# Kernel optimization log

Measured on AMD Instinct MI355X. Metric: run time of the kernel, lower is better.

Reference implementation:

```python
import jax, jax.numpy as jnp
import numpy as np

D_MODEL = 1024
D_INTERNAL = 64
SEQ = 2048
BATCH = 4


def setup_inputs() -> dict:
    key = jax.random.key(0)
    ks = jax.random.split(key, 9)
    s = 1.0 / np.sqrt(D_MODEL)
    return {
        "query": jax.random.normal(ks[0], (SEQ, BATCH, D_MODEL), jnp.float32),
        "key": jax.random.normal(ks[1], (SEQ, BATCH, D_MODEL), jnp.float32),
        "value": jax.random.normal(ks[2], (SEQ, BATCH, D_MODEL), jnp.float32),
        "Wq": jax.random.normal(ks[3], (D_MODEL, D_INTERNAL), jnp.float32) * s,
        "bq": jnp.zeros((D_INTERNAL,), jnp.float32),
        "Wk": jax.random.normal(ks[4], (D_MODEL, D_INTERNAL), jnp.float32) * s,
        "bk": jnp.zeros((D_INTERNAL,), jnp.float32),
        "Wv": jax.random.normal(ks[5], (D_MODEL, D_MODEL), jnp.float32) * s,
        "bv": jnp.zeros((D_MODEL,), jnp.float32),
    }


def reference(query, key, value, Wq, bq, Wk, bk, Wv, bv):
    # inputs: (S, B, D); project then move batch first -> (B, S, *)
    q = (query @ Wq + bq).transpose(1, 0, 2)          # (B, S, d_int)
    k = (key @ Wk + bk).transpose(1, 0, 2)            # (B, S, d_int)
    v = (value @ Wv + bv).transpose(1, 0, 2)          # (B, S, D)
    scores = jnp.einsum("bqd,bkd->bqk", q, k) / jnp.sqrt(jnp.float32(D_INTERNAL))
    probs = jax.nn.softmax(scores, axis=-1)           # row softmax over keys
    # extra renormalization over the QUERY axis (dim=1), as in the source
    probs = probs / (1e-9 + probs.sum(axis=1, keepdims=True))
    aten = jnp.einsum("bqk,bkd->bqd", probs, v).transpose(1, 0, 2)  # (S, B, D)
    return aten, probs
```

## Files before the change

### kernel.cpp

```cpp
#include <hip/hip_runtime.h>
#include <math.h>

#define SEQ 2048
#define BATCH 4
#define DM 1024
#define DI 64

typedef __attribute__((ext_vector_type(8))) short bf16x8;
typedef __attribute__((ext_vector_type(4))) float f32x4;

__device__ __forceinline__ unsigned short f2bf(float f) {
  unsigned u = __float_as_uint(f);
  unsigned r = (u + 0x7fff + ((u >> 16) & 1)) >> 16;
  return (unsigned short)r;
}

__device__ __forceinline__ void gload_lds16(const void* g, void* l) {
  __builtin_amdgcn_global_load_lds(
      (const __attribute__((address_space(1))) unsigned int*)g,
      (__attribute__((address_space(3))) unsigned int*)l, 16, 0, 0);
}


__global__ __launch_bounds__(256) void wqkt_kernel(
    const float* __restrict__ Wq, const float* __restrict__ Wk,
    unsigned short* __restrict__ WqkT) {
  __shared__ unsigned short t[64][65];
  const float* W = blockIdx.y ? Wk : Wq;
  unsigned short* WT = WqkT + (size_t)blockIdx.y * DI * DM;
  int bx = blockIdx.x * 64;
  int lx = threadIdx.x & 63, ly = threadIdx.x >> 6;
#pragma unroll
  for (int i = 0; i < 64; i += 4)
    t[ly + i][lx] = f2bf(W[(size_t)(bx + ly + i) * DI + lx]);
  __syncthreads();
#pragma unroll
  for (int i = 0; i < 64; i += 4)
    WT[(size_t)(ly + i) * DM + bx + lx] = t[lx][ly + i];
}

__global__ __launch_bounds__(256) void wvt_kernel(
    const float* __restrict__ W, unsigned short* __restrict__ WT) {
  __shared__ unsigned short t[64][65];
  int bx = blockIdx.x * 64, by = blockIdx.y * 64;
  int lx = threadIdx.x & 63, ly = threadIdx.x >> 6;
#pragma unroll
  for (int i = 0; i < 64; i += 4)
    t[ly + i][lx] = f2bf(W[(size_t)(bx + ly + i) * DM + by + lx]);
  __syncthreads();
#pragma unroll
  for (int i = 0; i < 64; i += 4)
    WT[(size_t)(by + ly + i) * DM + bx + lx] = t[lx][ly + i];
}

__global__ __launch_bounds__(256) void qkproj_mfma(
    const float* __restrict__ query, const float* __restrict__ key,
    const unsigned short* __restrict__ WqkT,
    const float* __restrict__ bq, const float* __restrict__ bk,
    unsigned short* __restrict__ qbf, unsigned short* __restrict__ kbf) {
  __shared__ __align__(16) unsigned short As[32 * 32];
  __shared__ __align__(16) unsigned short Bs[64 * 32];
  int which = blockIdx.y;
  const float* A = (which ? key : query) + (size_t)blockIdx.x * 32 * DM;
  const unsigned short* Bt = WqkT + (size_t)which * DI * DM;
  const float* bias = which ? bk : bq;
  unsigned short* outp = which ? kbf : qbf;

  const int tid = threadIdx.x;
  const int lane = tid & 63, wave = tid >> 6;
  const int lrow = lane & 15, quad = lane >> 4;
  const int wr = (wave >> 1) * 16;
  const int wc = (wave & 1) * 32;
  const int sw = (quad ^ ((lrow >> 1) & 3)) * 8;
  f32x4 acc[2] = {};

  const int am = tid >> 3, asub = tid & 7;
  const int akc = asub * 4;
  const int asl = am * 32 + (((asub >> 1) ^ ((am >> 1) & 3)) * 8) + (asub & 1) * 4;
  const int bn = tid >> 2;
  const int bkc = (((tid & 3) ^ ((bn >> 1) & 3)) * 8);

  for (int k0 = 0; k0 < DM; k0 += 32) {
    __syncthreads();
    gload_lds16(Bt + (size_t)bn * DM + k0 + bkc, Bs + wave * 512);
    float4 a = *(const float4*)(A + (size_t)am * DM + k0 + akc);
    ushort4 h;
    h.x = f2bf(a.x); h.y = f2bf(a.y); h.z = f2bf(a.z); h.w = f2bf(a.w);
    *(ushort4*)&As[asl] = h;
    __syncthreads();
    bf16x8 af = *(const bf16x8*)&As[(wr + lrow) * 32 + sw];
    bf16x8 b0 = *(const bf16x8*)&Bs[(wc + lrow) * 32 + sw];
    bf16x8 b1 = *(const bf16x8*)&Bs[(wc + 16 + lrow) * 32 + sw];
    acc[0] = __builtin_amdgcn_mfma_f32_16x16x32_bf16(af, b0, acc[0], 0, 0, 0);
    acc[1] = __builtin_amdgcn_mfma_f32_16x16x32_bf16(af, b1, acc[1], 0, 0, 0);
  }
  int sbase = blockIdx.x * 8 + (wr >> 2) + quad;
#pragma unroll
  for (int ni = 0; ni < 2; ++ni) {
    int n = wc + ni * 16 + lrow;
    float bb = bias[n];
#pragma unroll
    for (int reg = 0; reg < 4; ++reg)
      outp[((size_t)reg * SEQ + sbase) * DI + n] = f2bf(acc[ni][reg] + bb);
  }
}

__global__ __launch_bounds__(256) void vcast_kernel(
    const float* __restrict__ value, unsigned short* __restrict__ vbf) {
  size_t i = ((size_t)blockIdx.x * 256 + threadIdx.x) * 8;
  float4 a = *(const float4*)(value + i);
  float4 b = *(const float4*)(value + i + 4);
  bf16x8 h;
  h[0] = (short)f2bf(a.x); h[1] = (short)f2bf(a.y);
  h[2] = (short)f2bf(a.z); h[3] = (short)f2bf(a.w);
  h[4] = (short)f2bf(b.x); h[5] = (short)f2bf(b.y);
  h[6] = (short)f2bf(b.z); h[7] = (short)f2bf(b.w);
  *(bf16x8*)(vbf + i) = h;
}

__device__ __forceinline__ void mfma_core_bb(
    const unsigned short* __restrict__ At, int lda,
    const unsigned short* __restrict__ Bt, int ldb,
    int K, f32x4 (&acc)[4][4],
    unsigned short* As, unsigned short* Bs) {
  const int tid  = threadIdx.x;
  const int lane = tid & 63;
  const int wave = tid >> 6;
  const int wr   = (wave >> 1) * 64;
  const int wc   = (wave & 1) * 64;
  const int lrow = lane & 15;
  const int quad = lane >> 4;
  const int sw   = (quad ^ ((lrow >> 1) & 3)) * 8;

  for (int k0 = 0; k0 < K; k0 += 32) {
    __syncthreads();
#pragma unroll
    for (int it = 0; it < 2; ++it) {
      int c = it * 256 + wave * 64 + lane;
      int m = c >> 2, kc = ((c & 3) ^ ((c >> 3) & 3)) * 8;
      gload_lds16(At + (size_t)m * lda + k0 + kc,
                  As + (size_t)(it * 256 + wave * 64) * 8);
    }
#pragma unroll
    for (int it = 0; it < 2; ++it) {
      int c = it * 256 + wave * 64 + lane;
      int n = c >> 2, kc = ((c & 3) ^ ((c >> 3) & 3)) * 8;
      gload_lds16(Bt + (size_t)n * ldb + k0 + kc,
                  Bs + (size_t)(it * 256 + wave * 64) * 8);
    }
    __syncthreads();
    bf16x8 af[4], bfr[4];
#pragma unroll
    for (int mi = 0; mi < 4; ++mi)
      af[mi] = *(const bf16x8*)&As[(wr + mi * 16 + lrow) * 32 + sw];
#pragma unroll
    for (int ni = 0; ni < 4; ++ni)
      bfr[ni] = *(const bf16x8*)&Bs[(wc + ni * 16 + lrow) * 32 + sw];
#pragma unroll
    for (int mi = 0; mi < 4; ++mi)
#pragma unroll
      for (int ni = 0; ni < 4; ++ni)
        acc[mi][ni] = __builtin_amdgcn_mfma_f32_16x16x32_bf16(
            af[mi], bfr[ni], acc[mi][ni], 0, 0, 0);
  }
}

__device__ __forceinline__ void mfma_core_bb_12864(
    const unsigned short* __restrict__ At, int lda,
    const unsigned short* __restrict__ Bt, int ldb,
    int K, f32x4 (&acc)[4][2],
    unsigned short* As, unsigned short* Bs) {
  const int tid  = threadIdx.x;
  const int lane = tid & 63;
  const int wave = tid >> 6;
  const int wr   = (wave >> 1) * 64;
  const int wc   = (wave & 1) * 32;
  const int lrow = lane & 15;
  const int quad = lane >> 4;
  const int sw   = (quad ^ ((lrow >> 1) & 3)) * 8;
  const int bn   = tid >> 2;
  const int bkc  = ((tid & 3) ^ ((bn >> 1) & 3)) * 8;

  for (int k0 = 0; k0 < K; k0 += 32) {
    __syncthreads();
#pragma unroll
    for (int it = 0; it < 2; ++it) {
      int c = it * 256 + tid;
      int m = c >> 2, kc = ((c & 3) ^ ((m >> 1) & 3)) * 8;
      gload_lds16(At + (size_t)m * lda + k0 + kc,
                  As + (size_t)(it * 256 + wave * 64) * 8);
    }
    gload_lds16(Bt + (size_t)bn * ldb + k0 + bkc, Bs + wave * 512);
    __syncthreads();
    bf16x8 af[4], bfr[2];
#pragma unroll
    for (int mi = 0; mi < 4; ++mi)
      af[mi] = *(const bf16x8*)&As[(wr + mi * 16 + lrow) * 32 + sw];
#pragma unroll
    for (int ni = 0; ni < 2; ++ni)
      bfr[ni] = *(const bf16x8*)&Bs[(wc + ni * 16 + lrow) * 32 + sw];
#pragma unroll
    for (int mi = 0; mi < 4; ++mi)
#pragma unroll
      for (int ni = 0; ni < 2; ++ni)
        acc[mi][ni] = __builtin_amdgcn_mfma_f32_16x16x32_bf16(
            af[mi], bfr[ni], acc[mi][ni], 0, 0, 0);
  }
}

__global__ __launch_bounds__(256) void vproj_mfma(
    const unsigned short* __restrict__ vbf, const unsigned short* __restrict__ WvT,
    const float* __restrict__ bv, unsigned short* __restrict__ vT) {
  __shared__ __align__(16) unsigned short As[128 * 32];
  __shared__ __align__(16) unsigned short Bs[64 * 32];
  __shared__ __align__(16) unsigned short ep[64 * 4 * 32];
  f32x4 acc[4][2] = {};
  int m0 = blockIdx.x * 128, n0 = blockIdx.y * 64;
  mfma_core_bb_12864(vbf + (size_t)m0 * DM, DM, WvT + (size_t)n0 * DM, DM, DM,
                     acc, As, Bs);
  const int tid = threadIdx.x;
  const int lane = tid & 63, wave = tid >> 6;
  const int wr = (wave >> 1) * 64, wc = (wave & 1) * 32;
  const int lrow = lane & 15, quad = lane >> 4;
#pragma unroll
  for (int mi = 0; mi < 4; ++mi) {
    int ss = (wr >> 2) + mi * 4 + quad;
#pragma unroll
    for (int ni = 0; ni < 2; ++ni) {
      int nn = wc + ni * 16 + lrow;
      float bias = bv[n0 + nn];
      int swz = (nn & 3) << 3;
#pragma unroll
      for (int reg = 0; reg < 4; ++reg)
        ep[nn * 128 + reg * 32 + (ss ^ swz)] = f2bf(acc[mi][ni][reg] + bias);
    }
  }
  __syncthreads();
  int s0 = m0 >> 2;
#pragma unroll
  for (int t8 = 0; t8 < 4; ++t8) {
    int c = t8 * 256 + tid;
    int ss8 = (c & 3) * 8, b = (c >> 2) & 3, nn = c >> 4;
    uint4 vv = *(const uint4*)&ep[nn * 128 + b * 32 + (ss8 ^ ((nn & 3) << 3))];
    *(uint4*)&vT[((size_t)(b * DM + n0 + nn)) * SEQ + s0 + ss8] = vv;
  }
}

__global__ __launch_bounds__(256) void scores_mfma(
    const unsigned short* __restrict__ qbf, const unsigned short* __restrict__ kbf,
    float* __restrict__ probs) {
  __shared__ __align__(16) unsigned short As[128 * 32];
  __shared__ __align__(16) unsigned short Bs[128 * 32];
  int b = blockIdx.z;
  f32x4 acc[4][4] = {};
  mfma_core_bb(qbf + ((size_t)b * SEQ + blockIdx.x * 128) * DI, DI,
               kbf + ((size_t)b * SEQ + blockIdx.y * 128) * DI, DI, DI,
               acc, As, Bs);
  float* C = probs + (size_t)b * SEQ * SEQ;
  const int lane = threadIdx.x & 63, wave = threadIdx.x >> 6;
  const int wr = (wave >> 1) * 64, wc = (wave & 1) * 64;
  const int lrow = lane & 15, quad = lane >> 4;
#pragma unroll
  for (int mi = 0; mi < 4; ++mi) {
    int qr = blockIdx.x * 128 + wr + mi * 16 + quad * 4;
#pragma unroll
    for (int ni = 0; ni < 4; ++ni) {
      int n = blockIdx.y * 128 + wc + ni * 16 + lrow;
#pragma unroll
      for (int reg = 0; reg < 4; ++reg)
        C[(size_t)(qr + reg) * SEQ + n] = acc[mi][ni][reg] * 0.125f;
    }
  }
}

__global__ __launch_bounds__(256) void softmax_kernel(float* __restrict__ probs) {
  size_t row = (size_t)blockIdx.y * SEQ + blockIdx.x;
  float* p = probs + row * SEQ;
  int tid = threadIdx.x;
  float4 x0 = *(float4*)(p + tid * 4);
  float4 x1 = *(float4*)(p + 1024 + tid * 4);
  float m = fmaxf(fmaxf(fmaxf(x0.x, x0.y), fmaxf(x0.z, x0.w)),
                  fmaxf(fmaxf(x1.x, x1.y), fmaxf(x1.z, x1.w)));
  __shared__ float red[256];
  red[tid] = m;
  __syncthreads();
  for (int s2 = 128; s2 > 0; s2 >>= 1) {
    if (tid < s2) red[tid] = fmaxf(red[tid], red[tid + s2]);
    __syncthreads();
  }
  m = red[0];
  __syncthreads();
  x0.x = __expf(x0.x - m); x0.y = __expf(x0.y - m);
  x0.z = __expf(x0.z - m); x0.w = __expf(x0.w - m);
  x1.x = __expf(x1.x - m); x1.y = __expf(x1.y - m);
  x1.z = __expf(x1.z - m); x1.w = __expf(x1.w - m);
  float sum = x0.x + x0.y + x0.z + x0.w + x1.x + x1.y + x1.z + x1.w;
  red[tid] = sum;
  __syncthreads();
  for (int s2 = 128; s2 > 0; s2 >>= 1) {
    if (tid < s2) red[tid] += red[tid + s2];
    __syncthreads();
  }
  float inv = 1.0f / red[0];
  x0.x *= inv; x0.y *= inv; x0.z *= inv; x0.w *= inv;
  x1.x *= inv; x1.y *= inv; x1.z *= inv; x1.w *= inv;
  *(float4*)(p + tid * 4) = x0;
  *(float4*)(p + 1024 + tid * 4) = x1;
}

__global__ void zero_kernel(float* __restrict__ p, int n) {
  int i = blockIdx.x * blockDim.x + threadIdx.x;
  if (i < n) p[i] = 0.f;
}

__global__ __launch_bounds__(256) void colsum_kernel(
    const float* __restrict__ probs, float* __restrict__ colsum) {
  int b = blockIdx.z;
  int k = blockIdx.x * 256 + threadIdx.x;
  int q0 = blockIdx.y * 128;
  const float* p = probs + (size_t)b * SEQ * SEQ + (size_t)q0 * SEQ + k;
  float sum = 0.f;
#pragma unroll 4
  for (int i = 0; i < 128; ++i) sum += p[(size_t)i * SEQ];
  atomicAdd(&colsum[b * SEQ + k], sum);
}

__global__ void invcol_kernel(const float* __restrict__ colsum,
                              float* __restrict__ invcol, int n) {
  int i = blockIdx.x * blockDim.x + threadIdx.x;
  if (i < n) invcol[i] = 1.0f / (1e-9f + colsum[i]);
}

__global__ __launch_bounds__(256) void renorm_kernel(
    float* __restrict__ probs, const float* __restrict__ invcol,
    unsigned short* __restrict__ smb) {
  size_t i4 = (size_t)blockIdx.x * blockDim.x + threadIdx.x;
  size_t f = i4 * 4;
  int b = (int)(f >> 22);
  int k = (int)(f & 2047);
  float4 p = *(float4*)(probs + f);
  float4 c = *(const float4*)(invcol + b * SEQ + k);
  p.x *= c.x; p.y *= c.y; p.z *= c.z; p.w *= c.w;
  *(float4*)(probs + f) = p;
  ushort4 h;
  h.x = f2bf(p.x); h.y = f2bf(p.y); h.z = f2bf(p.z); h.w = f2bf(p.w);
  *(ushort4*)(smb + f) = h;
}

__global__ __launch_bounds__(256) void aten_mfma(
    const unsigned short* __restrict__ smb, const unsigned short* __restrict__ vT,
    float* __restrict__ out) {
  __shared__ __align__(16) unsigned short As[128 * 32];
  __shared__ __align__(16) unsigned short Bs[128 * 32];
  int b = blockIdx.z;
  f32x4 acc[4][4] = {};
  int m0 = blockIdx.x * 128, n0 = blockIdx.y * 128;
  mfma_core_bb(smb + ((size_t)b * SEQ + m0) * SEQ, SEQ,
               vT + ((size_t)b * DM + n0) * SEQ, SEQ, SEQ, acc, As, Bs);
  const int lane = threadIdx.x & 63, wave = threadIdx.x >> 6;
  const int wr = (wave >> 1) * 64, wc = (wave & 1) * 64;
  const int lrow = lane & 15, quad = lane >> 4;
#pragma unroll
  for (int mi = 0; mi < 4; ++mi) {
    int qr = m0 + wr + mi * 16 + quad * 4;
#pragma unroll
    for (int ni = 0; ni < 4; ++ni) {
      int n = n0 + wc + ni * 16 + lrow;
#pragma unroll
      for (int reg = 0; reg < 4; ++reg)
        out[(size_t)(qr + reg) * (BATCH * DM) + b * DM + n] = acc[mi][ni][reg];
    }
  }
}

extern "C" void kernel_launch(void* const* d_in, const int* in_sizes, int n_in,
                              void* d_out, int out_size, void* d_ws, size_t ws_size,
                              hipStream_t stream) {
  const float* query = (const float*)d_in[0];
  const float* key   = (const float*)d_in[1];
  const float* value = (const float*)d_in[2];
  const float* Wq    = (const float*)d_in[3];
  const float* bq    = (const float*)d_in[4];
  const float* Wk    = (const float*)d_in[5];
  const float* bk    = (const float*)d_in[6];
  const float* Wv    = (const float*)d_in[7];
  const float* bv    = (const float*)d_in[8];

  float* out   = (float*)d_out;
  float* probs = out + (size_t)SEQ * BATCH * DM;

  unsigned short* WvT  = (unsigned short*)d_ws;
  unsigned short* WqkT = WvT  + (size_t)DM * DM;
  unsigned short* qbf  = WqkT + (size_t)2 * DI * DM;
  unsigned short* kbf  = qbf  + (size_t)BATCH * SEQ * DI;
  unsigned short* vT   = kbf  + (size_t)BATCH * SEQ * DI;
  unsigned short* smb  = vT   + (size_t)BATCH * DM * SEQ;
  unsigned short* vbf  = smb;
  float* colsum = (float*)(smb + (size_t)BATCH * SEQ * SEQ);
  float* invcol = colsum + (size_t)BATCH * SEQ;

  wqkt_kernel<<<dim3(16, 2), 256, 0, stream>>>(Wq, Wk, WqkT);
  qkproj_mfma<<<dim3(SEQ * BATCH / 32, 2), 256, 0, stream>>>(
      query, key, WqkT, bq, bk, qbf, kbf);
  wvt_kernel<<<dim3(16, 16), 256, 0, stream>>>(Wv, WvT);
  vcast_kernel<<<(SEQ * BATCH * DM / 8) / 256, 256, 0, stream>>>(value, vbf);
  vproj_mfma<<<dim3(SEQ * BATCH / 128, DM / 64), 256, 0, stream>>>(vbf, WvT, bv, vT);
  scores_mfma<<<dim3(SEQ / 128, SEQ / 128, BATCH), 256, 0, stream>>>(qbf, kbf, probs);
  softmax_kernel<<<dim3(SEQ, BATCH), 256, 0, stream>>>(probs);
  zero_kernel<<<(BATCH * SEQ + 255) / 256, 256, 0, stream>>>(colsum, BATCH * SEQ);
  colsum_kernel<<<dim3(SEQ / 256, SEQ / 128, BATCH), 256, 0, stream>>>(probs, colsum);
  invcol_kernel<<<(BATCH * SEQ + 255) / 256, 256, 0, stream>>>(colsum, invcol, BATCH * SEQ);
  renorm_kernel<<<(BATCH * SEQ * SEQ / 4) / 256, 256, 0, stream>>>(probs, invcol, smb);
  aten_mfma<<<dim3(SEQ / 128, DM / 128, BATCH), 256, 0, stream>>>(smb, vT, out);
}
```

Before: 351.5 us.

## Fuse softmax exp and row sums into scores kernel, defer row normalization

```diff
diff --git a/kernel.cpp b/kernel.cpp
--- a/kernel.cpp
+++ b/kernel.cpp
@@ -248,7 +248,7 @@
 
 __global__ __launch_bounds__(256) void scores_mfma(
     const unsigned short* __restrict__ qbf, const unsigned short* __restrict__ kbf,
-    float* __restrict__ probs) {
+    float* __restrict__ probs, float* __restrict__ rowsum) {
   __shared__ __align__(16) unsigned short As[128 * 32];
   __shared__ __align__(16) unsigned short Bs[128 * 32];
   int b = blockIdx.z;
@@ -257,55 +257,42 @@
                kbf + ((size_t)b * SEQ + blockIdx.y * 128) * DI, DI, DI,
                acc, As, Bs);
   float* C = probs + (size_t)b * SEQ * SEQ;
+  float* rs = rowsum + (size_t)b * SEQ;
   const int lane = threadIdx.x & 63, wave = threadIdx.x >> 6;
   const int wr = (wave >> 1) * 64, wc = (wave & 1) * 64;
   const int lrow = lane & 15, quad = lane >> 4;
 #pragma unroll
   for (int mi = 0; mi < 4; ++mi) {
     int qr = blockIdx.x * 128 + wr + mi * 16 + quad * 4;
+    float r0 = 0.f, r1 = 0.f, r2 = 0.f, r3 = 0.f;
 #pragma unroll
     for (int ni = 0; ni < 4; ++ni) {
       int n = blockIdx.y * 128 + wc + ni * 16 + lrow;
-#pragma unroll
-      for (int reg = 0; reg < 4; ++reg)
-        C[(size_t)(qr + reg) * SEQ + n] = acc[mi][ni][reg] * 0.125f;
-    }
-  }
-}
-
-__global__ __launch_bounds__(256) void softmax_kernel(float* __restrict__ probs) {
-  size_t row = (size_t)blockIdx.y * SEQ + blockIdx.x;
-  float* p = probs + row * SEQ;
-  int tid = threadIdx.x;
-  float4 x0 = *(float4*)(p + tid * 4);
-  float4 x1 = *(float4*)(p + 1024 + tid * 4);
-  float m = fmaxf(fmaxf(fmaxf(x0.x, x0.y), fmaxf(x0.z, x0.w)),
-                  fmaxf(fmaxf(x1.x, x1.y), fmaxf(x1.z, x1.w)));
-  __shared__ float red[256];
-  red[tid] = m;
-  __syncthreads();
-  for (int s2 = 128; s2 > 0; s2 >>= 1) {
-    if (tid < s2) red[tid] = fmaxf(red[tid], red[tid + s2]);
-    __syncthreads();
-  }
-  m = red[0];
-  __syncthreads();
-  x0.x = __expf(x0.x - m); x0.y = __expf(x0.y - m);
-  x0.z = __expf(x0.z - m); x0.w = __expf(x0.w - m);
-  x1.x = __expf(x1.x - m); x1.y = __expf(x1.y - m);
-  x1.z = __expf(x1.z - m); x1.w = __expf(x1.w - m);
-  float sum = x0.x + x0.y + x0.z + x0.w + x1.x + x1.y + x1.z + x1.w;
-  red[tid] = sum;
-  __syncthreads();
-  for (int s2 = 128; s2 > 0; s2 >>= 1) {
-    if (tid < s2) red[tid] += red[tid + s2];
-    __syncthreads();
-  }
-  float inv = 1.0f / red[0];
-  x0.x *= inv; x0.y *= inv; x0.z *= inv; x0.w *= inv;
-  x1.x *= inv; x1.y *= inv; x1.z *= inv; x1.w *= inv;
-  *(float4*)(p + tid * 4) = x0;
-  *(float4*)(p + 1024 + tid * 4) = x1;
+      float e0 = __expf(acc[mi][ni][0] * 0.125f);
+      float e1 = __expf(acc[mi][ni][1] * 0.125f);
+      float e2 = __expf(acc[mi][ni][2] * 0.125f);
+      float e3 = __expf(acc[mi][ni][3] * 0.125f);
+      C[(size_t)(qr + 0) * SEQ + n] = e0;
+      C[(size_t)(qr + 1) * SEQ + n] = e1;
+      C[(size_t)(qr + 2) * SEQ + n] = e2;
+      C[(size_t)(qr + 3) * SEQ + n] = e3;
+      r0 += e0; r1 += e1; r2 += e2; r3 += e3;
+    }
+    r0 += __shfl_xor(r0, 1); r0 += __shfl_xor(r0, 2);
+    r0 += __shfl_xor(r0, 4); r0 += __shfl_xor(r0, 8);
+    r1 += __shfl_xor(r1, 1); r1 += __shfl_xor(r1, 2);
+    r1 += __shfl_xor(r1, 4); r1 += __shfl_xor(r1, 8);
+    r2 += __shfl_xor(r2, 1); r2 += __shfl_xor(r2, 2);
+    r2 += __shfl_xor(r2, 4); r2 += __shfl_xor(r2, 8);
+    r3 += __shfl_xor(r3, 1); r3 += __shfl_xor(r3, 2);
+    r3 += __shfl_xor(r3, 4); r3 += __shfl_xor(r3, 8);
+    if (lrow == 0) {
+      atomicAdd(&rs[qr + 0], r0);
+      atomicAdd(&rs[qr + 1], r1);
+      atomicAdd(&rs[qr + 2], r2);
+      atomicAdd(&rs[qr + 3], r3);
+    }
+  }
 }
 
 __global__ void zero_kernel(float* __restrict__ p, int n) {
@@ -313,34 +300,38 @@
   if (i < n) p[i] = 0.f;
 }
 
+__global__ void recip_kernel(const float* __restrict__ in,
+                             float* __restrict__ outp, float eps, int n) {
+  int i = blockIdx.x * blockDim.x + threadIdx.x;
+  if (i < n) outp[i] = 1.0f / (eps + in[i]);
+}
+
 __global__ __launch_bounds__(256) void colsum_kernel(
-    const float* __restrict__ probs, float* __restrict__ colsum) {
+    const float* __restrict__ probs, const float* __restrict__ invrs,
+    float* __restrict__ colsum) {
   int b = blockIdx.z;
   int k = blockIdx.x * 256 + threadIdx.x;
   int q0 = blockIdx.y * 128;
   const float* p = probs + (size_t)b * SEQ * SEQ + (size_t)q0 * SEQ + k;
+  const float* ir = invrs + (size_t)b * SEQ + q0;
   float sum = 0.f;
 #pragma unroll 4
-  for (int i = 0; i < 128; ++i) sum += p[(size_t)i * SEQ];
+  for (int i = 0; i < 128; ++i) sum += p[(size_t)i * SEQ] * ir[i];
   atomicAdd(&colsum[b * SEQ + k], sum);
 }
 
-__global__ void invcol_kernel(const float* __restrict__ colsum,
-                              float* __restrict__ invcol, int n) {
-  int i = blockIdx.x * blockDim.x + threadIdx.x;
-  if (i < n) invcol[i] = 1.0f / (1e-9f + colsum[i]);
-}
-
 __global__ __launch_bounds__(256) void renorm_kernel(
-    float* __restrict__ probs, const float* __restrict__ invcol,
-    unsigned short* __restrict__ smb) {
+    float* __restrict__ probs, const float* __restrict__ invrs,
+    const float* __restrict__ invcol, unsigned short* __restrict__ smb) {
   size_t i4 = (size_t)blockIdx.x * blockDim.x + threadIdx.x;
   size_t f = i4 * 4;
   int b = (int)(f >> 22);
+  int q = (int)((f >> 11) & 2047);
   int k = (int)(f & 2047);
+  float ir = invrs[b * SEQ + q];
   float4 p = *(float4*)(probs + f);
   float4 c = *(const float4*)(invcol + b * SEQ + k);
-  p.x *= c.x; p.y *= c.y; p.z *= c.z; p.w *= c.w;
+  p.x *= ir * c.x; p.y *= ir * c.y; p.z *= ir * c.z; p.w *= ir * c.w;
   *(float4*)(probs + f) = p;
   ushort4 h;
   h.x = f2bf(p.x); h.y = f2bf(p.y); h.z = f2bf(p.z); h.w = f2bf(p.w);
@@ -352,9 +343,11 @@
     float* __restrict__ out) {
   __shared__ __align__(16) unsigned short As[128 * 32];
   __shared__ __align__(16) unsigned short Bs[128 * 32];
-  int b = blockIdx.z;
+  int bid = blockIdx.x;
+  int wg = (bid & 7) * 64 + (bid >> 3);
+  int mb = wg & 15, nb = (wg >> 4) & 7, b = wg >> 7;
   f32x4 acc[4][4] = {};
-  int m0 = blockIdx.x * 128, n0 = blockIdx.y * 128;
+  int m0 = mb * 128, n0 = nb * 128;
   mfma_core_bb(smb + ((size_t)b * SEQ + m0) * SEQ, SEQ,
                vT + ((size_t)b * DM + n0) * SEQ, SEQ, SEQ, acc, As, Bs);
   const int lane = threadIdx.x & 63, wave = threadIdx.x >> 6;
@@ -396,8 +389,10 @@
   unsigned short* vT   = kbf  + (size_t)BATCH * SEQ * DI;
   unsigned short* smb  = vT   + (size_t)BATCH * DM * SEQ;
   unsigned short* vbf  = smb;
-  float* colsum = (float*)(smb + (size_t)BATCH * SEQ * SEQ);
-  float* invcol = colsum + (size_t)BATCH * SEQ;
+  float* rowsum = (float*)(smb + (size_t)BATCH * SEQ * SEQ);
+  float* colsum = rowsum + (size_t)BATCH * SEQ;
+  float* invrs  = colsum + (size_t)BATCH * SEQ;
+  float* invcol = invrs  + (size_t)BATCH * SEQ;
 
   wqkt_kernel<<<dim3(16, 2), 256, 0, stream>>>(Wq, Wk, WqkT);
   qkproj_mfma<<<dim3(SEQ * BATCH / 32, 2), 256, 0, stream>>>(
@@ -405,11 +400,16 @@
   wvt_kernel<<<dim3(16, 16), 256, 0, stream>>>(Wv, WvT);
   vcast_kernel<<<(SEQ * BATCH * DM / 8) / 256, 256, 0, stream>>>(value, vbf);
   vproj_mfma<<<dim3(SEQ * BATCH / 128, DM / 64), 256, 0, stream>>>(vbf, WvT, bv, vT);
-  scores_mfma<<<dim3(SEQ / 128, SEQ / 128, BATCH), 256, 0, stream>>>(qbf, kbf, probs);
-  softmax_kernel<<<dim3(SEQ, BATCH), 256, 0, stream>>>(probs);
-  zero_kernel<<<(BATCH * SEQ + 255) / 256, 256, 0, stream>>>(colsum, BATCH * SEQ);
-  colsum_kernel<<<dim3(SEQ / 256, SEQ / 128, BATCH), 256, 0, stream>>>(probs, colsum);
-  invcol_kernel<<<(BATCH * SEQ + 255) / 256, 256, 0, stream>>>(colsum, invcol, BATCH * SEQ);
-  renorm_kernel<<<(BATCH * SEQ * SEQ / 4) / 256, 256, 0, stream>>>(probs, invcol, smb);
-  aten_mfma<<<dim3(SEQ / 128, DM / 128, BATCH), 256, 0, stream>>>(smb, vT, out);
-}
+  zero_kernel<<<(2 * BATCH * SEQ + 255) / 256, 256, 0, stream>>>(rowsum, 2 * BATCH * SEQ);
+  scores_mfma<<<dim3(SEQ / 128, SEQ / 128, BATCH), 256, 0, stream>>>(
+      qbf, kbf, probs, rowsum);
+  recip_kernel<<<(BATCH * SEQ + 255) / 256, 256, 0, stream>>>(
+      rowsum, invrs, 0.0f, BATCH * SEQ);
+  colsum_kernel<<<dim3(SEQ / 256, SEQ / 128, BATCH), 256, 0, stream>>>(
+      probs, invrs, colsum);
+  recip_kernel<<<(BATCH * SEQ + 255) / 256, 256, 0, stream>>>(
+      colsum, invcol, 1e-9f, BATCH * SEQ);
+  renorm_kernel<<<(BATCH * SEQ * SEQ / 4) / 256, 256, 0, stream>>>(
+      probs, invrs, invcol, smb);
+  aten_mfma<<<dim3(512), 256, 0, stream>>>(smb, vT, out);
+}
```

New measurement: 335.1 us. 4.7% less time.
